# Kernel tuning notes

Hardware: AMD Instinct MI355X
Metric: run time of the kernel (lower is better)

Reference implementation:

```python
import jax, jax.numpy as jnp
import numpy as np

N = 500_000
LEVELS = 3
GDIM = 8
BASE_H = 128
BASE_W = 128
COND = 64
DOUT = 128
HID = 2
DIN = 1 + 2 * LEVELS * GDIM  # rho + theta-grid feats + rho-grid feats = 49


def _bilinear(grid, u, v):
    # grid: [H, W, D]; u, v in [0,1]; u indexes W axis, v indexes H axis.
    H, W, D = grid.shape
    x = u * (W - 1)
    y = v * (H - 1)
    x0 = jnp.clip(jnp.floor(x).astype(jnp.int32), 0, W - 2)
    y0 = jnp.clip(jnp.floor(y).astype(jnp.int32), 0, H - 2)
    x1 = x0 + 1
    y1 = y0 + 1
    wx = (x - x0)[:, None]
    wy = (y - y0)[:, None]
    g = grid.reshape(H * W, D)
    c00 = jnp.take(g, y0 * W + x0, axis=0)
    c01 = jnp.take(g, y0 * W + x1, axis=0)
    c10 = jnp.take(g, y1 * W + x0, axis=0)
    c11 = jnp.take(g, y1 * W + x1, axis=0)
    return (c00 * (1 - wx) * (1 - wy) + c01 * wx * (1 - wy)
            + c10 * (1 - wx) * wy + c11 * wx * wy)


def setup_inputs() -> dict:
    key = jax.random.key(0)
    ks = jax.random.split(key, 24)
    inp = {
        'coords': jax.random.uniform(ks[0], (N,), dtype=jnp.float32),
        'angles': jax.random.uniform(ks[1], (N,), dtype=jnp.float32),
        'rho': jax.random.normal(ks[2], (N,), dtype=jnp.float32),
        'rho_n': jax.random.uniform(ks[3], (N,), dtype=jnp.float32),
        'curve_feats': jax.random.normal(ks[4], (N, COND), dtype=jnp.float32),
        'type_sample': jax.random.normal(ks[5], (N, DOUT), dtype=jnp.float32),
    }
    # Multi-resolution grids (theta-conditioned and rho-conditioned).
    for l in range(LEVELS):
        h, w = BASE_H * 2 ** l, BASE_W * 2 ** l
        inp[f'gt{l}'] = 0.1 * jax.random.normal(ks[6 + l], (h, w, GDIM), dtype=jnp.float32)
        inp[f'gr{l}'] = 0.1 * jax.random.normal(ks[9 + l], (h, w, GDIM), dtype=jnp.float32)
    # FiLM-modulated encoder chain (block 0 + HID residual blocks).
    inp['film0_fcW'] = jax.random.normal(ks[12], (DIN, DOUT), dtype=jnp.float32) / np.sqrt(DIN)
    inp['film0_fcb'] = jnp.zeros((DOUT,), dtype=jnp.float32)
    inp['filmh_fcW'] = jax.random.normal(ks[13], (HID, DOUT, DOUT), dtype=jnp.float32) / np.sqrt(DOUT)
    inp['filmh_fcb'] = jnp.zeros((HID, DOUT), dtype=jnp.float32)
    inp['gammaW'] = 0.02 * jax.random.normal(ks[14], (HID + 1, COND, DOUT), dtype=jnp.float32)
    inp['gammab'] = jnp.ones((HID + 1, DOUT), dtype=jnp.float32)
    inp['betaW'] = 0.02 * jax.random.normal(ks[15], (HID + 1, COND, DOUT), dtype=jnp.float32)
    inp['betab'] = jnp.zeros((HID + 1, DOUT), dtype=jnp.float32)
    # Decoder MLP [DOUT, 64, 1].
    inp['decW1'] = jax.random.normal(ks[16], (DOUT, 64), dtype=jnp.float32) / np.sqrt(DOUT)
    inp['decb1'] = jnp.zeros((64,), dtype=jnp.float32)
    inp['decW2'] = jax.random.normal(ks[17], (64, 1), dtype=jnp.float32) / 8.0
    inp['decb2'] = jnp.zeros((1,), dtype=jnp.float32)
    return inp


def reference(coords, angles, rho, rho_n, curve_feats, type_sample,
              gt0, gt1, gt2, gr0, gr1, gr2,
              film0_fcW, film0_fcb, filmh_fcW, filmh_fcb,
              gammaW, gammab, betaW, betab,
              decW1, decb1, decW2, decb2):
    # Multi-res grid interpolation, concat across levels.
    ct = jnp.concatenate([_bilinear(g, angles, coords) for g in (gt0, gt1, gt2)], axis=-1)
    cr = jnp.concatenate([_bilinear(g, rho_n, coords) for g in (gr0, gr1, gr2)], axis=-1)
    feat = jnp.concatenate([rho[:, None], ct, cr], axis=-1)  # [N, DIN]
    # FiLM conditioning: gamma/beta per block from curve_feats.
    gamma = jnp.einsum('nc,lcd->lnd', curve_feats, gammaW) + gammab[:, None, :]
    beta = jnp.einsum('nc,lcd->lnd', curve_feats, betaW) + betab[:, None, :]
    # Block 0 + type_sample residual.
    x = jax.nn.silu(gamma[0] * (feat @ film0_fcW + film0_fcb) + beta[0]) + type_sample
    # Residual FiLM blocks.
    for i in range(filmh_fcW.shape[0]):
        x = x + jax.nn.silu(gamma[i + 1] * (x @ filmh_fcW[i] + filmh_fcb[i]) + beta[i + 1])
    # Decoder MLP.
    h = jax.nn.relu(x @ decW1 + decb1)
    sdf = (h @ decW2 + decb2)[..., 0]  # [N]
    return sdf
```

## Files before the change

### kernel.cpp

```cpp
#include <hip/hip_runtime.h>
#include <stdint.h>

typedef short s16x8 __attribute__((ext_vector_type(8)));
typedef short s16x4 __attribute__((ext_vector_type(4)));
typedef float f32x4 __attribute__((ext_vector_type(4)));

#define MFMA16(a, b, c) __builtin_amdgcn_mfma_f32_16x16x32_bf16(a, b, c, 0, 0, 0)

__device__ __forceinline__ short f2bf(float f) {
  uint32_t u = __builtin_bit_cast(uint32_t, f);
  u += 0x7FFFu + ((u >> 16) & 1u);
  return (short)(u >> 16);
}

__global__ void pack_w(const float* __restrict__ w0, const float* __restrict__ wh,
                       const float* __restrict__ gw, const float* __restrict__ bw,
                       const float* __restrict__ d1, short* __restrict__ out) {
  int idx = blockIdx.x * 512 + threadIdx.x;
  if (idx >= 98304) return;
  int f = idx >> 9;
  int r = idx & 511;
  int lane = r >> 3, e = r & 7;
  int kk = ((lane >> 4) << 3) + e;
  int nn = lane & 15;
  float v;
  if (f < 16) {
    int ct = f >> 1, ks = f & 1;
    int k = ks * 32 + kk, n = ct * 16 + nn;
    if (k < 48) v = w0[(1 + k) * 128 + n];
    else if (k == 48) v = w0[n];
    else v = 0.f;
  } else if (f < 112) {
    int f2 = f - 16;
    int ks = f2 & 1, ct = (f2 >> 1) & 7, gb = (f2 >> 4) & 1, l = f2 >> 5;
    int k = ks * 32 + kk, n = ct * 16 + nn;
    const float* Wp = gb ? bw : gw;
    v = Wp[(l * 64 + k) * 128 + n];
  } else if (f < 176) {
    int f2 = f - 112;
    int ks = f2 & 3, ct = (f2 >> 2) & 7, i = f2 >> 5;
    int k = ks * 32 + kk, n = ct * 16 + nn;
    v = wh[(i * 128 + k) * 128 + n];
  } else {
    int f2 = f - 176;
    int ks = f2 & 3, ct = f2 >> 2;
    int k = ks * 32 + kk, n = ct * 16 + nn;
    v = d1[k * 64 + n];
  }
  out[idx] = f2bf(v);
}

__global__ __launch_bounds__(512) void ngc_main(
    const float* __restrict__ coords, const float* __restrict__ angles,
    const float* __restrict__ rho, const float* __restrict__ rho_n,
    const float* __restrict__ cf, const float* __restrict__ ts,
    const float* __restrict__ gt0, const float* __restrict__ gr0,
    const float* __restrict__ gt1, const float* __restrict__ gr1,
    const float* __restrict__ gt2, const float* __restrict__ gr2,
    const float* __restrict__ f0b, const float* __restrict__ fhb,
    const float* __restrict__ gab, const float* __restrict__ beb,
    const float* __restrict__ d1b, const float* __restrict__ d2w,
    const float* __restrict__ d2b, const short* __restrict__ pw,
    float* __restrict__ out, int n) {
  __shared__ __align__(16) char smem[33 * 1024];
  char* featA = smem;
  char* cfA   = smem + 8 * 1024;
  char* xA    = smem + 16 * 1024;
  float* red  = (float*)(smem + 32 * 1024);

  const int tid = threadIdx.x;
  const int lane = tid & 63;
  const int w = tid >> 6;
  const int g16 = lane >> 4;
  const int l15 = lane & 15;
  const int row0 = blockIdx.x * 64;
  const int col = w * 16 + l15;
  const int cbase = col >> 5;
  const int cslot = ((col >> 3) & 3) * 16;
  const int ce = (col & 7) * 2;

  float tsr[4][4];
#pragma unroll
  for (int rg = 0; rg < 4; ++rg)
#pragma unroll
    for (int rr = 0; rr < 4; ++rr) {
      int grow = row0 + rg * 16 + g16 * 4 + rr; grow = grow < n ? grow : n - 1;
      tsr[rg][rr] = ts[(size_t)grow * 128 + col];
    }

  if (tid < 384) {
    int r = tid & 63, g = tid >> 6;
    int gr_ = row0 + r; gr_ = gr_ < n ? gr_ : n - 1;
    float vv = coords[gr_];
    float u = (g < 3) ? angles[gr_] : rho_n[gr_];
    int lvl = (g < 3) ? g : g - 3;
    const float* G = (g == 0) ? gt0 : (g == 1) ? gt1 : (g == 2) ? gt2
                   : (g == 3) ? gr0 : (g == 4) ? gr1 : gr2;
    int Wg = 128 << lvl;
    float x = u * (float)(Wg - 1), y = vv * (float)(Wg - 1);
    int ix = (int)x; ix = ix < 0 ? 0 : (ix > Wg - 2 ? Wg - 2 : ix);
    int iy = (int)y; iy = iy < 0 ? 0 : (iy > Wg - 2 ? Wg - 2 : iy);
    float wx = x - (float)ix, wy = y - (float)iy;
    const float4* p0 = (const float4*)(G + (size_t)(iy * Wg + ix) * 8);
    const float4* p1 = (const float4*)(G + (size_t)((iy + 1) * Wg + ix) * 8);
    float4 c00a = p0[0], c00b = p0[1], c01a = p0[2], c01b = p0[3];
    float4 c10a = p1[0], c10b = p1[1], c11a = p1[2], c11b = p1[3];
    float w00 = (1.f - wx) * (1.f - wy), w01 = wx * (1.f - wy);
    float w10 = (1.f - wx) * wy, w11 = wx * wy;
    s16x8 o;
    o[0] = f2bf(c00a.x * w00 + c01a.x * w01 + c10a.x * w10 + c11a.x * w11);
    o[1] = f2bf(c00a.y * w00 + c01a.y * w01 + c10a.y * w10 + c11a.y * w11);
    o[2] = f2bf(c00a.z * w00 + c01a.z * w01 + c10a.z * w10 + c11a.z * w11);
    o[3] = f2bf(c00a.w * w00 + c01a.w * w01 + c10a.w * w10 + c11a.w * w11);
    o[4] = f2bf(c00b.x * w00 + c01b.x * w01 + c10b.x * w10 + c11b.x * w11);
    o[5] = f2bf(c00b.y * w00 + c01b.y * w01 + c10b.y * w10 + c11b.y * w11);
    o[6] = f2bf(c00b.z * w00 + c01b.z * w01 + c10b.z * w10 + c11b.z * w11);
    o[7] = f2bf(c00b.w * w00 + c01b.w * w01 + c10b.w * w10 + c11b.w * w11);
    int dst16 = ((r >> 4) * 2 + (g >> 2)) * 64 + (g & 3) * 16 + (r & 15);
    *(s16x8*)(featA + dst16 * 16) = o;
  }

  {
    int cb = tid & 7, r = tid >> 3;
    int gr_ = row0 + r; gr_ = gr_ < n ? gr_ : n - 1;
    const float4* cp = (const float4*)(cf + (size_t)gr_ * 64 + cb * 8);
    float4 v0 = cp[0], v1 = cp[1];
    s16x8 s = { f2bf(v0.x), f2bf(v0.y), f2bf(v0.z), f2bf(v0.w),
                f2bf(v1.x), f2bf(v1.y), f2bf(v1.z), f2bf(v1.w) };
    int dst16 = ((r >> 4) * 2 + (cb >> 2)) * 64 + (cb & 3) * 16 + (r & 15);
    *(s16x8*)(cfA + dst16 * 16) = s;
  }

  if (tid < 64) {
    int r = tid;
    int gr_ = row0 + r; gr_ = gr_ < n ? gr_ : n - 1;
    s16x8 a = { f2bf(rho[gr_]), 0, 0, 0, 0, 0, 0, 0 };
    s16x8 z = { 0, 0, 0, 0, 0, 0, 0, 0 };
    int base = ((r >> 4) * 2 + 1) * 64;
    *(s16x8*)(featA + (base + 32 + (r & 15)) * 16) = a;
    *(s16x8*)(featA + (base + 48 + (r & 15)) * 16) = z;
  }
  __syncthreads();

  auto ldF = [&](const char* b, int frag) -> s16x8 {
    return *(const s16x8*)(b + (frag * 64 + lane) * 16);
  };
  auto ldw = [&](int frag) -> s16x8 { return ((const s16x8*)pw)[frag * 64 + lane]; };

  float xr[4][4];

  {
    s16x8 bw0 = ldw(w * 2), bw1 = ldw(w * 2 + 1);
    s16x8 bg0 = ldw(16 + w * 2), bg1 = ldw(16 + w * 2 + 1);
    s16x8 bb0 = ldw(32 + w * 2), bb1 = ldw(32 + w * 2 + 1);
    float f0bv = f0b[col], gabv = gab[col], bebv = beb[col];
#pragma unroll
    for (int rg = 0; rg < 4; ++rg) {
      s16x8 a0 = ldF(featA, rg * 2), a1 = ldF(featA, rg * 2 + 1);
      s16x8 c0 = ldF(cfA, rg * 2), c1 = ldF(cfA, rg * 2 + 1);
      f32x4 t = {0.f, 0.f, 0.f, 0.f};
      t = MFMA16(a0, bw0, t); t = MFMA16(a1, bw1, t);
      f32x4 ga = {0.f, 0.f, 0.f, 0.f};
      ga = MFMA16(c0, bg0, ga); ga = MFMA16(c1, bg1, ga);
      f32x4 be = {0.f, 0.f, 0.f, 0.f};
      be = MFMA16(c0, bb0, be); be = MFMA16(c1, bb1, be);
      char* xbase = xA + (rg * 4 + cbase) * 1024 + ce;
#pragma unroll
      for (int rr = 0; rr < 4; ++rr) {
        float z = (ga[rr] + gabv) * (t[rr] + f0bv) + (be[rr] + bebv);
        float sl = z * __builtin_amdgcn_rcpf(1.f + __expf(-z));
        xr[rg][rr] = sl + tsr[rg][rr];
        *(short*)(xbase + (cslot + g16 * 4 + rr) * 16) = f2bf(xr[rg][rr]);
      }
    }
  }
  __syncthreads();

#pragma unroll
  for (int i = 0; i < 2; ++i) {
    s16x8 bh0 = ldw(112 + i * 32 + w * 4);
    s16x8 bh1 = ldw(112 + i * 32 + w * 4 + 1);
    s16x8 bh2 = ldw(112 + i * 32 + w * 4 + 2);
    s16x8 bh3 = ldw(112 + i * 32 + w * 4 + 3);
    s16x8 bg0 = ldw(16 + (i + 1) * 32 + w * 2);
    s16x8 bg1 = ldw(16 + (i + 1) * 32 + w * 2 + 1);
    s16x8 bb0 = ldw(16 + (i + 1) * 32 + 16 + w * 2);
    s16x8 bb1 = ldw(16 + (i + 1) * 32 + 16 + w * 2 + 1);
    float fhbv = fhb[i * 128 + col];
    float gabv = gab[(i + 1) * 128 + col];
    float bebv = beb[(i + 1) * 128 + col];
    f32x4 zs[4];
#pragma unroll
    for (int rg = 0; rg < 4; ++rg) {
      s16x8 xa = ldF(xA, rg * 4), xb = ldF(xA, rg * 4 + 1);
      s16x8 xc = ldF(xA, rg * 4 + 2), xd = ldF(xA, rg * 4 + 3);
      s16x8 c0 = ldF(cfA, rg * 2), c1 = ldF(cfA, rg * 2 + 1);
      f32x4 t = {0.f, 0.f, 0.f, 0.f};
      t = MFMA16(xa, bh0, t); t = MFMA16(xb, bh1, t);
      t = MFMA16(xc, bh2, t); t = MFMA16(xd, bh3, t);
      f32x4 ga = {0.f, 0.f, 0.f, 0.f};
      ga = MFMA16(c0, bg0, ga); ga = MFMA16(c1, bg1, ga);
      f32x4 be = {0.f, 0.f, 0.f, 0.f};
      be = MFMA16(c0, bb0, be); be = MFMA16(c1, bb1, be);
      f32x4 z;
#pragma unroll
      for (int rr = 0; rr < 4; ++rr) {
        float zz = (ga[rr] + gabv) * (t[rr] + fhbv) + (be[rr] + bebv);
        z[rr] = zz * __builtin_amdgcn_rcpf(1.f + __expf(-zz));
      }
      zs[rg] = z;
    }
    __syncthreads();
#pragma unroll
    for (int rg = 0; rg < 4; ++rg) {
      char* xbase = xA + (rg * 4 + cbase) * 1024 + ce;
#pragma unroll
      for (int rr = 0; rr < 4; ++rr) {
        xr[rg][rr] += zs[rg][rr];
        *(short*)(xbase + (cslot + g16 * 4 + rr) * 16) = f2bf(xr[rg][rr]);
      }
    }
    __syncthreads();
  }

  {
    int ctd = w & 3, rbase = (w >> 2) * 2;
    int dcol = ctd * 16 + l15;
    s16x8 bd0 = ldw(176 + ctd * 4), bd1 = ldw(176 + ctd * 4 + 1);
    s16x8 bd2 = ldw(176 + ctd * 4 + 2), bd3 = ldw(176 + ctd * 4 + 3);
    float d1bv = d1b[dcol], w2v = d2w[dcol];
#pragma unroll
    for (int q = 0; q < 2; ++q) {
      int rg = rbase + q;
      s16x8 xa = ldF(xA, rg * 4), xb = ldF(xA, rg * 4 + 1);
      s16x8 xc = ldF(xA, rg * 4 + 2), xd = ldF(xA, rg * 4 + 3);
      f32x4 hh = {0.f, 0.f, 0.f, 0.f};
      hh = MFMA16(xa, bd0, hh); hh = MFMA16(xb, bd1, hh);
      hh = MFMA16(xc, bd2, hh); hh = MFMA16(xd, bd3, hh);
#pragma unroll
      for (int rr = 0; rr < 4; ++rr) {
        float h = fmaxf(hh[rr] + d1bv, 0.f) * w2v;
        h += __shfl_xor(h, 1);
        h += __shfl_xor(h, 2);
        h += __shfl_xor(h, 4);
        h += __shfl_xor(h, 8);
        if (l15 == 0) red[(rg * 16 + g16 * 4 + rr) * 4 + ctd] = h;
      }
    }
  }
  __syncthreads();
  if (tid < 64) {
    int grow = row0 + tid;
    if (grow < n)
      out[grow] = red[tid * 4 + 0] + red[tid * 4 + 1] + red[tid * 4 + 2] +
                  red[tid * 4 + 3] + d2b[0];
  }
}

extern "C" void kernel_launch(void* const* d_in, const int* in_sizes, int n_in,
                              void* d_out, int out_size, void* d_ws, size_t ws_size,
                              hipStream_t stream) {
  int n = in_sizes[0];
  short* pw = (short*)d_ws;
  pack_w<<<192, 512, 0, stream>>>(
      (const float*)d_in[12],
      (const float*)d_in[14],
      (const float*)d_in[16],
      (const float*)d_in[18],
      (const float*)d_in[20],
      pw);
  int nb = (n + 63) / 64;
  ngc_main<<<nb, 512, 0, stream>>>(
      (const float*)d_in[0],
      (const float*)d_in[1],
      (const float*)d_in[2],
      (const float*)d_in[3],
      (const float*)d_in[4],
      (const float*)d_in[5],
      (const float*)d_in[6],
      (const float*)d_in[7],
      (const float*)d_in[8],
      (const float*)d_in[9],
      (const float*)d_in[10],
      (const float*)d_in[11],
      (const float*)d_in[13],
      (const float*)d_in[15],
      (const float*)d_in[17],
      (const float*)d_in[19],
      (const float*)d_in[21],
      (const float*)d_in[22],
      (const float*)d_in[23],
      pw, (float*)d_out, n);
}
```

Measured before the change: 259.6 us.

## Make main kernel persistent with register prefetch of next tile inputs

Launches a fixed grid of at most 512 blocks that stride over the 64-row tiles instead of one block per tile. While the current tile computes, each block loads the next tile's coordinates, angles, rho, curve features and type_sample rows into registers, so global latency overlaps with the MFMA stages. The cost is fewer resident blocks per CU, which means less latency hiding through occupancy, plus some load imbalance because the tile count does not divide evenly by the grid size. Register pressure also rises from holding the prefetched values.

Result: slower. 284.4 us (+9.6%).

```diff
diff --git a/kernel.cpp b/kernel.cpp
--- a/kernel.cpp
+++ b/kernel.cpp
@@ -2,10 +2,10 @@
 #include <stdint.h>
 
 typedef short s16x8 __attribute__((ext_vector_type(8)));
-typedef short s16x4 __attribute__((ext_vector_type(4)));
 typedef float f32x4 __attribute__((ext_vector_type(4)));
 
 #define MFMA16(a, b, c) __builtin_amdgcn_mfma_f32_16x16x32_bf16(a, b, c, 0, 0, 0)
+#define NBLK 512
 
 __device__ __forceinline__ short f2bf(float f) {
   uint32_t u = __builtin_bit_cast(uint32_t, f);
@@ -61,7 +61,7 @@
     const float* __restrict__ gab, const float* __restrict__ beb,
     const float* __restrict__ d1b, const float* __restrict__ d2w,
     const float* __restrict__ d2b, const short* __restrict__ pw,
-    float* __restrict__ out, int n) {
+    float* __restrict__ out, int n, int ntiles) {
   __shared__ __align__(16) char smem[33 * 1024];
   char* featA = smem;
   char* cfA   = smem + 8 * 1024;
@@ -73,187 +73,207 @@
   const int w = tid >> 6;
   const int g16 = lane >> 4;
   const int l15 = lane & 15;
-  const int row0 = blockIdx.x * 64;
   const int col = w * 16 + l15;
   const int cbase = col >> 5;
   const int cslot = ((col >> 3) & 3) * 16;
   const int ce = (col & 7) * 2;
 
+  const int r_g = tid & 63;
+  const int g_id = tid >> 6;
+  const int r_cf = tid >> 3;
+  const int cb = tid & 7;
+
+  float c_, a_, rn_, rhov;
+  float4 cf0, cf1;
   float tsr[4][4];
-#pragma unroll
-  for (int rg = 0; rg < 4; ++rg)
-#pragma unroll
-    for (int rr = 0; rr < 4; ++rr) {
-      int grow = row0 + rg * 16 + g16 * 4 + rr; grow = grow < n ? grow : n - 1;
-      tsr[rg][rr] = ts[(size_t)grow * 128 + col];
-    }
-
-  if (tid < 384) {
-    int r = tid & 63, g = tid >> 6;
-    int gr_ = row0 + r; gr_ = gr_ < n ? gr_ : n - 1;
-    float vv = coords[gr_];
-    float u = (g < 3) ? angles[gr_] : rho_n[gr_];
-    int lvl = (g < 3) ? g : g - 3;
-    const float* G = (g == 0) ? gt0 : (g == 1) ? gt1 : (g == 2) ? gt2
-                   : (g == 3) ? gr0 : (g == 4) ? gr1 : gr2;
-    int Wg = 128 << lvl;
-    float x = u * (float)(Wg - 1), y = vv * (float)(Wg - 1);
-    int ix = (int)x; ix = ix < 0 ? 0 : (ix > Wg - 2 ? Wg - 2 : ix);
-    int iy = (int)y; iy = iy < 0 ? 0 : (iy > Wg - 2 ? Wg - 2 : iy);
-    float wx = x - (float)ix, wy = y - (float)iy;
-    const float4* p0 = (const float4*)(G + (size_t)(iy * Wg + ix) * 8);
-    const float4* p1 = (const float4*)(G + (size_t)((iy + 1) * Wg + ix) * 8);
-    float4 c00a = p0[0], c00b = p0[1], c01a = p0[2], c01b = p0[3];
-    float4 c10a = p1[0], c10b = p1[1], c11a = p1[2], c11b = p1[3];
-    float w00 = (1.f - wx) * (1.f - wy), w01 = wx * (1.f - wy);
-    float w10 = (1.f - wx) * wy, w11 = wx * wy;
-    s16x8 o;
-    o[0] = f2bf(c00a.x * w00 + c01a.x * w01 + c10a.x * w10 + c11a.x * w11);
-    o[1] = f2bf(c00a.y * w00 + c01a.y * w01 + c10a.y * w10 + c11a.y * w11);
-    o[2] = f2bf(c00a.z * w00 + c01a.z * w01 + c10a.z * w10 + c11a.z * w11);
-    o[3] = f2bf(c00a.w * w00 + c01a.w * w01 + c10a.w * w10 + c11a.w * w11);
-    o[4] = f2bf(c00b.x * w00 + c01b.x * w01 + c10b.x * w10 + c11b.x * w11);
-    o[5] = f2bf(c00b.y * w00 + c01b.y * w01 + c10b.y * w10 + c11b.y * w11);
-    o[6] = f2bf(c00b.z * w00 + c01b.z * w01 + c10b.z * w10 + c11b.z * w11);
-    o[7] = f2bf(c00b.w * w00 + c01b.w * w01 + c10b.w * w10 + c11b.w * w11);
-    int dst16 = ((r >> 4) * 2 + (g >> 2)) * 64 + (g & 3) * 16 + (r & 15);
-    *(s16x8*)(featA + dst16 * 16) = o;
-  }
-
-  {
-    int cb = tid & 7, r = tid >> 3;
-    int gr_ = row0 + r; gr_ = gr_ < n ? gr_ : n - 1;
-    const float4* cp = (const float4*)(cf + (size_t)gr_ * 64 + cb * 8);
-    float4 v0 = cp[0], v1 = cp[1];
-    s16x8 s = { f2bf(v0.x), f2bf(v0.y), f2bf(v0.z), f2bf(v0.w),
-                f2bf(v1.x), f2bf(v1.y), f2bf(v1.z), f2bf(v1.w) };
-    int dst16 = ((r >> 4) * 2 + (cb >> 2)) * 64 + (cb & 3) * 16 + (r & 15);
-    *(s16x8*)(cfA + dst16 * 16) = s;
-  }
-
-  if (tid < 64) {
-    int r = tid;
-    int gr_ = row0 + r; gr_ = gr_ < n ? gr_ : n - 1;
-    s16x8 a = { f2bf(rho[gr_]), 0, 0, 0, 0, 0, 0, 0 };
-    s16x8 z = { 0, 0, 0, 0, 0, 0, 0, 0 };
-    int base = ((r >> 4) * 2 + 1) * 64;
-    *(s16x8*)(featA + (base + 32 + (r & 15)) * 16) = a;
-    *(s16x8*)(featA + (base + 48 + (r & 15)) * 16) = z;
-  }
-  __syncthreads();
+
+  auto issueA = [&](int tt) {
+    int row0 = tt * 64;
+    int gr1 = row0 + r_g; gr1 = gr1 < n ? gr1 : n - 1;
+    c_ = coords[gr1]; a_ = angles[gr1]; rn_ = rho_n[gr1]; rhov = rho[gr1];
+    int gr2 = row0 + r_cf; gr2 = gr2 < n ? gr2 : n - 1;
+    const float4* cp = (const float4*)(cf + (size_t)gr2 * 64 + cb * 8);
+    cf0 = cp[0]; cf1 = cp[1];
+  };
+  auto issueT = [&](int tt) {
+    int row0 = tt * 64;
+#pragma unroll
+    for (int rg = 0; rg < 4; ++rg)
+#pragma unroll
+      for (int rr = 0; rr < 4; ++rr) {
+        int grow = row0 + rg * 16 + g16 * 4 + rr; grow = grow < n ? grow : n - 1;
+        tsr[rg][rr] = ts[(size_t)grow * 128 + col];
+      }
+  };
 
   auto ldF = [&](const char* b, int frag) -> s16x8 {
     return *(const s16x8*)(b + (frag * 64 + lane) * 16);
   };
   auto ldw = [&](int frag) -> s16x8 { return ((const s16x8*)pw)[frag * 64 + lane]; };
 
-  float xr[4][4];
-
-  {
-    s16x8 bw0 = ldw(w * 2), bw1 = ldw(w * 2 + 1);
-    s16x8 bg0 = ldw(16 + w * 2), bg1 = ldw(16 + w * 2 + 1);
-    s16x8 bb0 = ldw(32 + w * 2), bb1 = ldw(32 + w * 2 + 1);
-    float f0bv = f0b[col], gabv = gab[col], bebv = beb[col];
-#pragma unroll
-    for (int rg = 0; rg < 4; ++rg) {
-      s16x8 a0 = ldF(featA, rg * 2), a1 = ldF(featA, rg * 2 + 1);
-      s16x8 c0 = ldF(cfA, rg * 2), c1 = ldF(cfA, rg * 2 + 1);
-      f32x4 t = {0.f, 0.f, 0.f, 0.f};
-      t = MFMA16(a0, bw0, t); t = MFMA16(a1, bw1, t);
-      f32x4 ga = {0.f, 0.f, 0.f, 0.f};
-      ga = MFMA16(c0, bg0, ga); ga = MFMA16(c1, bg1, ga);
-      f32x4 be = {0.f, 0.f, 0.f, 0.f};
-      be = MFMA16(c0, bb0, be); be = MFMA16(c1, bb1, be);
-      char* xbase = xA + (rg * 4 + cbase) * 1024 + ce;
-#pragma unroll
-      for (int rr = 0; rr < 4; ++rr) {
-        float z = (ga[rr] + gabv) * (t[rr] + f0bv) + (be[rr] + bebv);
-        float sl = z * __builtin_amdgcn_rcpf(1.f + __expf(-z));
-        xr[rg][rr] = sl + tsr[rg][rr];
-        *(short*)(xbase + (cslot + g16 * 4 + rr) * 16) = f2bf(xr[rg][rr]);
-      }
-    }
-  }
-  __syncthreads();
-
-#pragma unroll
-  for (int i = 0; i < 2; ++i) {
-    s16x8 bh0 = ldw(112 + i * 32 + w * 4);
-    s16x8 bh1 = ldw(112 + i * 32 + w * 4 + 1);
-    s16x8 bh2 = ldw(112 + i * 32 + w * 4 + 2);
-    s16x8 bh3 = ldw(112 + i * 32 + w * 4 + 3);
-    s16x8 bg0 = ldw(16 + (i + 1) * 32 + w * 2);
-    s16x8 bg1 = ldw(16 + (i + 1) * 32 + w * 2 + 1);
-    s16x8 bb0 = ldw(16 + (i + 1) * 32 + 16 + w * 2);
-    s16x8 bb1 = ldw(16 + (i + 1) * 32 + 16 + w * 2 + 1);
-    float fhbv = fhb[i * 128 + col];
-    float gabv = gab[(i + 1) * 128 + col];
-    float bebv = beb[(i + 1) * 128 + col];
-    f32x4 zs[4];
-#pragma unroll
-    for (int rg = 0; rg < 4; ++rg) {
-      s16x8 xa = ldF(xA, rg * 4), xb = ldF(xA, rg * 4 + 1);
-      s16x8 xc = ldF(xA, rg * 4 + 2), xd = ldF(xA, rg * 4 + 3);
-      s16x8 c0 = ldF(cfA, rg * 2), c1 = ldF(cfA, rg * 2 + 1);
-      f32x4 t = {0.f, 0.f, 0.f, 0.f};
-      t = MFMA16(xa, bh0, t); t = MFMA16(xb, bh1, t);
-      t = MFMA16(xc, bh2, t); t = MFMA16(xd, bh3, t);
-      f32x4 ga = {0.f, 0.f, 0.f, 0.f};
-      ga = MFMA16(c0, bg0, ga); ga = MFMA16(c1, bg1, ga);
-      f32x4 be = {0.f, 0.f, 0.f, 0.f};
-      be = MFMA16(c0, bb0, be); be = MFMA16(c1, bb1, be);
-      f32x4 z;
-#pragma unroll
-      for (int rr = 0; rr < 4; ++rr) {
-        float zz = (ga[rr] + gabv) * (t[rr] + fhbv) + (be[rr] + bebv);
-        z[rr] = zz * __builtin_amdgcn_rcpf(1.f + __expf(-zz));
-      }
-      zs[rg] = z;
-    }
+  int t = blockIdx.x;
+  issueA(t);
+  issueT(t);
+
+  for (; t < ntiles; t += NBLK) {
+    const int row0 = t * 64;
+
+    if (tid < 384) {
+      int r = r_g, g = g_id;
+      float u = (g < 3) ? a_ : rn_;
+      int lvl = (g < 3) ? g : g - 3;
+      const float* G = (g == 0) ? gt0 : (g == 1) ? gt1 : (g == 2) ? gt2
+                     : (g == 3) ? gr0 : (g == 4) ? gr1 : gr2;
+      int Wg = 128 << lvl;
+      float x = u * (float)(Wg - 1), y = c_ * (float)(Wg - 1);
+      int ix = (int)x; ix = ix < 0 ? 0 : (ix > Wg - 2 ? Wg - 2 : ix);
+      int iy = (int)y; iy = iy < 0 ? 0 : (iy > Wg - 2 ? Wg - 2 : iy);
+      float wx = x - (float)ix, wy = y - (float)iy;
+      const float4* p0 = (const float4*)(G + (size_t)(iy * Wg + ix) * 8);
+      const float4* p1 = (const float4*)(G + (size_t)((iy + 1) * Wg + ix) * 8);
+      float4 c00a = p0[0], c00b = p0[1], c01a = p0[2], c01b = p0[3];
+      float4 c10a = p1[0], c10b = p1[1], c11a = p1[2], c11b = p1[3];
+      float w00 = (1.f - wx) * (1.f - wy), w01 = wx * (1.f - wy);
+      float w10 = (1.f - wx) * wy, w11 = wx * wy;
+      s16x8 o;
+      o[0] = f2bf(c00a.x * w00 + c01a.x * w01 + c10a.x * w10 + c11a.x * w11);
+      o[1] = f2bf(c00a.y * w00 + c01a.y * w01 + c10a.y * w10 + c11a.y * w11);
+      o[2] = f2bf(c00a.z * w00 + c01a.z * w01 + c10a.z * w10 + c11a.z * w11);
+      o[3] = f2bf(c00a.w * w00 + c01a.w * w01 + c10a.w * w10 + c11a.w * w11);
+      o[4] = f2bf(c00b.x * w00 + c01b.x * w01 + c10b.x * w10 + c11b.x * w11);
+      o[5] = f2bf(c00b.y * w00 + c01b.y * w01 + c10b.y * w10 + c11b.y * w11);
+      o[6] = f2bf(c00b.z * w00 + c01b.z * w01 + c10b.z * w10 + c11b.z * w11);
+      o[7] = f2bf(c00b.w * w00 + c01b.w * w01 + c10b.w * w10 + c11b.w * w11);
+      int dst16 = ((r >> 4) * 2 + (g >> 2)) * 64 + (g & 3) * 16 + (r & 15);
+      *(s16x8*)(featA + dst16 * 16) = o;
+    }
+    {
+      s16x8 s = { f2bf(cf0.x), f2bf(cf0.y), f2bf(cf0.z), f2bf(cf0.w),
+                  f2bf(cf1.x), f2bf(cf1.y), f2bf(cf1.z), f2bf(cf1.w) };
+      int dst16 = ((r_cf >> 4) * 2 + (cb >> 2)) * 64 + (cb & 3) * 16 + (r_cf & 15);
+      *(s16x8*)(cfA + dst16 * 16) = s;
+    }
+    if (tid < 64) {
+      int r = tid;
+      s16x8 a = { f2bf(rhov), 0, 0, 0, 0, 0, 0, 0 };
+      s16x8 z = { 0, 0, 0, 0, 0, 0, 0, 0 };
+      int base = ((r >> 4) * 2 + 1) * 64;
+      *(s16x8*)(featA + (base + 32 + (r & 15)) * 16) = a;
+      *(s16x8*)(featA + (base + 48 + (r & 15)) * 16) = z;
+    }
+    int tn = t + NBLK;
+    if (tn < ntiles) issueA(tn);
     __syncthreads();
-#pragma unroll
-    for (int rg = 0; rg < 4; ++rg) {
-      char* xbase = xA + (rg * 4 + cbase) * 1024 + ce;
-#pragma unroll
-      for (int rr = 0; rr < 4; ++rr) {
-        xr[rg][rr] += zs[rg][rr];
-        *(short*)(xbase + (cslot + g16 * 4 + rr) * 16) = f2bf(xr[rg][rr]);
-      }
-    }
+
+    float xr[4][4];
+
+    {
+      s16x8 bw0 = ldw(w * 2), bw1 = ldw(w * 2 + 1);
+      s16x8 bg0 = ldw(16 + w * 2), bg1 = ldw(16 + w * 2 + 1);
+      s16x8 bb0 = ldw(32 + w * 2), bb1 = ldw(32 + w * 2 + 1);
+      float f0bv = f0b[col], gabv = gab[col], bebv = beb[col];
+#pragma unroll
+      for (int rg = 0; rg < 4; ++rg) {
+        s16x8 a0 = ldF(featA, rg * 2), a1 = ldF(featA, rg * 2 + 1);
+        s16x8 c0 = ldF(cfA, rg * 2), c1 = ldF(cfA, rg * 2 + 1);
+        f32x4 tt = {0.f, 0.f, 0.f, 0.f};
+        tt = MFMA16(a0, bw0, tt); tt = MFMA16(a1, bw1, tt);
+        f32x4 ga = {0.f, 0.f, 0.f, 0.f};
+        ga = MFMA16(c0, bg0, ga); ga = MFMA16(c1, bg1, ga);
+        f32x4 be = {0.f, 0.f, 0.f, 0.f};
+        be = MFMA16(c0, bb0, be); be = MFMA16(c1, bb1, be);
+        char* xbase = xA + (rg * 4 + cbase) * 1024 + ce;
+#pragma unroll
+        for (int rr = 0; rr < 4; ++rr) {
+          float z = (ga[rr] + gabv) * (tt[rr] + f0bv) + (be[rr] + bebv);
+          float sl = z * __builtin_amdgcn_rcpf(1.f + __expf(-z));
+          xr[rg][rr] = sl + tsr[rg][rr];
+          *(short*)(xbase + (cslot + g16 * 4 + rr) * 16) = f2bf(xr[rg][rr]);
+        }
+      }
+    }
+    if (tn < ntiles) issueT(tn);
     __syncthreads();
-  }
-
-  {
-    int ctd = w & 3, rbase = (w >> 2) * 2;
-    int dcol = ctd * 16 + l15;
-    s16x8 bd0 = ldw(176 + ctd * 4), bd1 = ldw(176 + ctd * 4 + 1);
-    s16x8 bd2 = ldw(176 + ctd * 4 + 2), bd3 = ldw(176 + ctd * 4 + 3);
-    float d1bv = d1b[dcol], w2v = d2w[dcol];
-#pragma unroll
-    for (int q = 0; q < 2; ++q) {
-      int rg = rbase + q;
-      s16x8 xa = ldF(xA, rg * 4), xb = ldF(xA, rg * 4 + 1);
-      s16x8 xc = ldF(xA, rg * 4 + 2), xd = ldF(xA, rg * 4 + 3);
-      f32x4 hh = {0.f, 0.f, 0.f, 0.f};
-      hh = MFMA16(xa, bd0, hh); hh = MFMA16(xb, bd1, hh);
-      hh = MFMA16(xc, bd2, hh); hh = MFMA16(xd, bd3, hh);
-#pragma unroll
-      for (int rr = 0; rr < 4; ++rr) {
-        float h = fmaxf(hh[rr] + d1bv, 0.f) * w2v;
-        h += __shfl_xor(h, 1);
-        h += __shfl_xor(h, 2);
-        h += __shfl_xor(h, 4);
-        h += __shfl_xor(h, 8);
-        if (l15 == 0) red[(rg * 16 + g16 * 4 + rr) * 4 + ctd] = h;
-      }
-    }
-  }
-  __syncthreads();
-  if (tid < 64) {
-    int grow = row0 + tid;
-    if (grow < n)
-      out[grow] = red[tid * 4 + 0] + red[tid * 4 + 1] + red[tid * 4 + 2] +
-                  red[tid * 4 + 3] + d2b[0];
+
+#pragma unroll
+    for (int i = 0; i < 2; ++i) {
+      s16x8 bh0 = ldw(112 + i * 32 + w * 4);
+      s16x8 bh1 = ldw(112 + i * 32 + w * 4 + 1);
+      s16x8 bh2 = ldw(112 + i * 32 + w * 4 + 2);
+      s16x8 bh3 = ldw(112 + i * 32 + w * 4 + 3);
+      s16x8 bg0 = ldw(16 + (i + 1) * 32 + w * 2);
+      s16x8 bg1 = ldw(16 + (i + 1) * 32 + w * 2 + 1);
+      s16x8 bb0 = ldw(16 + (i + 1) * 32 + 16 + w * 2);
+      s16x8 bb1 = ldw(16 + (i + 1) * 32 + 16 + w * 2 + 1);
+      float fhbv = fhb[i * 128 + col];
+      float gabv = gab[(i + 1) * 128 + col];
+      float bebv = beb[(i + 1) * 128 + col];
+      f32x4 zs[4];
+#pragma unroll
+      for (int rg = 0; rg < 4; ++rg) {
+        s16x8 xa = ldF(xA, rg * 4), xb = ldF(xA, rg * 4 + 1);
+        s16x8 xc = ldF(xA, rg * 4 + 2), xd = ldF(xA, rg * 4 + 3);
+        s16x8 c0 = ldF(cfA, rg * 2), c1 = ldF(cfA, rg * 2 + 1);
+        f32x4 tt = {0.f, 0.f, 0.f, 0.f};
+        tt = MFMA16(xa, bh0, tt); tt = MFMA16(xb, bh1, tt);
+        tt = MFMA16(xc, bh2, tt); tt = MFMA16(xd, bh3, tt);
+        f32x4 ga = {0.f, 0.f, 0.f, 0.f};
+        ga = MFMA16(c0, bg0, ga); ga = MFMA16(c1, bg1, ga);
+        f32x4 be = {0.f, 0.f, 0.f, 0.f};
+        be = MFMA16(c0, bb0, be); be = MFMA16(c1, bb1, be);
+        f32x4 z;
+#pragma unroll
+        for (int rr = 0; rr < 4; ++rr) {
+          float zz = (ga[rr] + gabv) * (tt[rr] + fhbv) + (be[rr] + bebv);
+          z[rr] = zz * __builtin_amdgcn_rcpf(1.f + __expf(-zz));
+        }
+        zs[rg] = z;
+      }
+      __syncthreads();
+#pragma unroll
+      for (int rg = 0; rg < 4; ++rg) {
+        char* xbase = xA + (rg * 4 + cbase) * 1024 + ce;
+#pragma unroll
+        for (int rr = 0; rr < 4; ++rr) {
+          xr[rg][rr] += zs[rg][rr];
+          *(short*)(xbase + (cslot + g16 * 4 + rr) * 16) = f2bf(xr[rg][rr]);
+        }
+      }
+      __syncthreads();
+    }
+
+    {
+      int ctd = w & 3, rbase = (w >> 2) * 2;
+      int dcol = ctd * 16 + l15;
+      s16x8 bd0 = ldw(176 + ctd * 4), bd1 = ldw(176 + ctd * 4 + 1);
+      s16x8 bd2 = ldw(176 + ctd * 4 + 2), bd3 = ldw(176 + ctd * 4 + 3);
+      float d1bv = d1b[dcol], w2v = d2w[dcol];
+#pragma unroll
+      for (int q = 0; q < 2; ++q) {
+        int rg = rbase + q;
+        s16x8 xa = ldF(xA, rg * 4), xb = ldF(xA, rg * 4 + 1);
+        s16x8 xc = ldF(xA, rg * 4 + 2), xd = ldF(xA, rg * 4 + 3);
+        f32x4 hh = {0.f, 0.f, 0.f, 0.f};
+        hh = MFMA16(xa, bd0, hh); hh = MFMA16(xb, bd1, hh);
+        hh = MFMA16(xc, bd2, hh); hh = MFMA16(xd, bd3, hh);
+#pragma unroll
+        for (int rr = 0; rr < 4; ++rr) {
+          float h = fmaxf(hh[rr] + d1bv, 0.f) * w2v;
+          h += __shfl_xor(h, 1);
+          h += __shfl_xor(h, 2);
+          h += __shfl_xor(h, 4);
+          h += __shfl_xor(h, 8);
+          if (l15 == 0) red[(rg * 16 + g16 * 4 + rr) * 4 + ctd] = h;
+        }
+      }
+    }
+    __syncthreads();
+    if (tid < 64) {
+      int grow = row0 + tid;
+      if (grow < n)
+        out[grow] = red[tid * 4 + 0] + red[tid * 4 + 1] + red[tid * 4 + 2] +
+                    red[tid * 4 + 3] + d2b[0];
+    }
   }
 }
 
@@ -269,7 +289,8 @@
       (const float*)d_in[18],
       (const float*)d_in[20],
       pw);
-  int nb = (n + 63) / 64;
+  int ntiles = (n + 63) / 64;
+  int nb = ntiles < NBLK ? ntiles : NBLK;
   ngc_main<<<nb, 512, 0, stream>>>(
       (const float*)d_in[0],
       (const float*)d_in[1],
@@ -290,5 +311,5 @@
       (const float*)d_in[21],
       (const float*)d_in[22],
       (const float*)d_in[23],
-      pw, (float*)d_out, n);
+      pw, (float*)d_out, n, ntiles);
 }
```

## Split grid gather into separate kernel staging bf16 features in workspace

Applied to the files above, without the earlier changes.

The fused kernel is split in two. One kernel does the bilinear grid gathers and writes bf16 feature fragments to a global workspace buffer; a second kernel reads them directly as MFMA operands and runs the FiLM/MLP GEMM chain. The launches are issued in chunks sized to the available workspace. The split is meant to separate the latency-bound random gathers from the MFMA work, freeing LDS and improving occupancy of each kernel. Separately, the manual bf16 rounding is replaced with the packed v_cvt_pk_bf16_f32 instruction. The cost is an extra global write and read of the features plus more kernel launches.

Measured after the change: 284.5 us. +9.6%, slower.

```diff
diff --git a/kernel.cpp b/kernel.cpp
--- a/kernel.cpp
+++ b/kernel.cpp
@@ -2,8 +2,8 @@
 #include <stdint.h>
 
 typedef short s16x8 __attribute__((ext_vector_type(8)));
-typedef short s16x4 __attribute__((ext_vector_type(4)));
 typedef float f32x4 __attribute__((ext_vector_type(4)));
+typedef uint32_t u32x4 __attribute__((ext_vector_type(4)));
 
 #define MFMA16(a, b, c) __builtin_amdgcn_mfma_f32_16x16x32_bf16(a, b, c, 0, 0, 0)
 
@@ -12,6 +12,12 @@
   u += 0x7FFFu + ((u >> 16) & 1u);
   return (short)(u >> 16);
 }
+__device__ __forceinline__ uint32_t cvtpk(float lo, float hi) {
+  uint32_t r;
+  asm("v_cvt_pk_bf16_f32 %0, %1, %2" : "=v"(r) : "v"(lo), "v"(hi));
+  return r;
+}
+__device__ __forceinline__ short f2bf1(float f) { return (short)cvtpk(f, f); }
 
 __global__ void pack_w(const float* __restrict__ w0, const float* __restrict__ wh,
                        const float* __restrict__ gw, const float* __restrict__ bw,
@@ -50,43 +56,16 @@
   out[idx] = f2bf(v);
 }
 
-__global__ __launch_bounds__(512) void ngc_main(
+__global__ __launch_bounds__(512) void ngc_gather(
     const float* __restrict__ coords, const float* __restrict__ angles,
     const float* __restrict__ rho, const float* __restrict__ rho_n,
-    const float* __restrict__ cf, const float* __restrict__ ts,
     const float* __restrict__ gt0, const float* __restrict__ gr0,
     const float* __restrict__ gt1, const float* __restrict__ gr1,
     const float* __restrict__ gt2, const float* __restrict__ gr2,
-    const float* __restrict__ f0b, const float* __restrict__ fhb,
-    const float* __restrict__ gab, const float* __restrict__ beb,
-    const float* __restrict__ d1b, const float* __restrict__ d2w,
-    const float* __restrict__ d2b, const short* __restrict__ pw,
-    float* __restrict__ out, int n) {
-  __shared__ __align__(16) char smem[33 * 1024];
-  char* featA = smem;
-  char* cfA   = smem + 8 * 1024;
-  char* xA    = smem + 16 * 1024;
-  float* red  = (float*)(smem + 32 * 1024);
-
+    short* __restrict__ stage, int n, int t0) {
   const int tid = threadIdx.x;
-  const int lane = tid & 63;
-  const int w = tid >> 6;
-  const int g16 = lane >> 4;
-  const int l15 = lane & 15;
-  const int row0 = blockIdx.x * 64;
-  const int col = w * 16 + l15;
-  const int cbase = col >> 5;
-  const int cslot = ((col >> 3) & 3) * 16;
-  const int ce = (col & 7) * 2;
-
-  float tsr[4][4];
-#pragma unroll
-  for (int rg = 0; rg < 4; ++rg)
-#pragma unroll
-    for (int rr = 0; rr < 4; ++rr) {
-      int grow = row0 + rg * 16 + g16 * 4 + rr; grow = grow < n ? grow : n - 1;
-      tsr[rg][rr] = ts[(size_t)grow * 128 + col];
-    }
+  const int row0 = (t0 + blockIdx.x) * 64;
+  char* st = (char*)(stage + (size_t)blockIdx.x * 4096);
 
   if (tid < 384) {
     int r = tid & 63, g = tid >> 6;
@@ -107,41 +86,77 @@
     float4 c10a = p1[0], c10b = p1[1], c11a = p1[2], c11b = p1[3];
     float w00 = (1.f - wx) * (1.f - wy), w01 = wx * (1.f - wy);
     float w10 = (1.f - wx) * wy, w11 = wx * wy;
-    s16x8 o;
-    o[0] = f2bf(c00a.x * w00 + c01a.x * w01 + c10a.x * w10 + c11a.x * w11);
-    o[1] = f2bf(c00a.y * w00 + c01a.y * w01 + c10a.y * w10 + c11a.y * w11);
-    o[2] = f2bf(c00a.z * w00 + c01a.z * w01 + c10a.z * w10 + c11a.z * w11);
-    o[3] = f2bf(c00a.w * w00 + c01a.w * w01 + c10a.w * w10 + c11a.w * w11);
-    o[4] = f2bf(c00b.x * w00 + c01b.x * w01 + c10b.x * w10 + c11b.x * w11);
-    o[5] = f2bf(c00b.y * w00 + c01b.y * w01 + c10b.y * w10 + c11b.y * w11);
-    o[6] = f2bf(c00b.z * w00 + c01b.z * w01 + c10b.z * w10 + c11b.z * w11);
-    o[7] = f2bf(c00b.w * w00 + c01b.w * w01 + c10b.w * w10 + c11b.w * w11);
+    float e0 = c00a.x * w00 + c01a.x * w01 + c10a.x * w10 + c11a.x * w11;
+    float e1 = c00a.y * w00 + c01a.y * w01 + c10a.y * w10 + c11a.y * w11;
+    float e2 = c00a.z * w00 + c01a.z * w01 + c10a.z * w10 + c11a.z * w11;
+    float e3 = c00a.w * w00 + c01a.w * w01 + c10a.w * w10 + c11a.w * w11;
+    float e4 = c00b.x * w00 + c01b.x * w01 + c10b.x * w10 + c11b.x * w11;
+    float e5 = c00b.y * w00 + c01b.y * w01 + c10b.y * w10 + c11b.y * w11;
+    float e6 = c00b.z * w00 + c01b.z * w01 + c10b.z * w10 + c11b.z * w11;
+    float e7 = c00b.w * w00 + c01b.w * w01 + c10b.w * w10 + c11b.w * w11;
+    u32x4 o = { cvtpk(e0, e1), cvtpk(e2, e3), cvtpk(e4, e5), cvtpk(e6, e7) };
     int dst16 = ((r >> 4) * 2 + (g >> 2)) * 64 + (g & 3) * 16 + (r & 15);
-    *(s16x8*)(featA + dst16 * 16) = o;
-  }
+    *(u32x4*)(st + dst16 * 16) = o;
+  } else if (tid < 448) {
+    int r = tid - 384;
+    int gr_ = row0 + r; gr_ = gr_ < n ? gr_ : n - 1;
+    s16x8 a = { f2bf1(rho[gr_]), 0, 0, 0, 0, 0, 0, 0 };
+    int base = ((r >> 4) * 2 + 1) * 64;
+    *(s16x8*)(st + (base + 32 + (r & 15)) * 16) = a;
+  } else {
+    int r = tid - 448;
+    s16x8 z = { 0, 0, 0, 0, 0, 0, 0, 0 };
+    int base = ((r >> 4) * 2 + 1) * 64;
+    *(s16x8*)(st + (base + 48 + (r & 15)) * 16) = z;
+  }
+}
+
+__global__ __launch_bounds__(512) void ngc_gemm(
+    const float* __restrict__ cf, const float* __restrict__ ts,
+    const float* __restrict__ f0b, const float* __restrict__ fhb,
+    const float* __restrict__ gab, const float* __restrict__ beb,
+    const float* __restrict__ d1b, const float* __restrict__ d2w,
+    const float* __restrict__ d2b, const short* __restrict__ pw,
+    const short* __restrict__ stage, float* __restrict__ out, int n, int t0) {
+  __shared__ __align__(16) char smem[25 * 1024];
+  char* cfA = smem;
+  char* xA  = smem + 8 * 1024;
+  float* red = (float*)(smem + 24 * 1024);
+
+  const int tid = threadIdx.x;
+  const int lane = tid & 63;
+  const int w = tid >> 6;
+  const int g16 = lane >> 4;
+  const int l15 = lane & 15;
+  const int row0 = (t0 + blockIdx.x) * 64;
+  const int col = w * 16 + l15;
+  const int cbase = col >> 5;
+  const int cslot = ((col >> 3) & 3) * 16;
+  const int ce = (col & 7) * 2;
+
+  float tsr[4][4];
+#pragma unroll
+  for (int rg = 0; rg < 4; ++rg)
+#pragma unroll
+    for (int rr = 0; rr < 4; ++rr) {
+      int grow = row0 + rg * 16 + g16 * 4 + rr; grow = grow < n ? grow : n - 1;
+      tsr[rg][rr] = ts[(size_t)grow * 128 + col];
+    }
 
   {
     int cb = tid & 7, r = tid >> 3;
     int gr_ = row0 + r; gr_ = gr_ < n ? gr_ : n - 1;
     const float4* cp = (const float4*)(cf + (size_t)gr_ * 64 + cb * 8);
     float4 v0 = cp[0], v1 = cp[1];
-    s16x8 s = { f2bf(v0.x), f2bf(v0.y), f2bf(v0.z), f2bf(v0.w),
-                f2bf(v1.x), f2bf(v1.y), f2bf(v1.z), f2bf(v1.w) };
+    u32x4 s = { cvtpk(v0.x, v0.y), cvtpk(v0.z, v0.w),
+                cvtpk(v1.x, v1.y), cvtpk(v1.z, v1.w) };
     int dst16 = ((r >> 4) * 2 + (cb >> 2)) * 64 + (cb & 3) * 16 + (r & 15);
-    *(s16x8*)(cfA + dst16 * 16) = s;
-  }
-
-  if (tid < 64) {
-    int r = tid;
-    int gr_ = row0 + r; gr_ = gr_ < n ? gr_ : n - 1;
-    s16x8 a = { f2bf(rho[gr_]), 0, 0, 0, 0, 0, 0, 0 };
-    s16x8 z = { 0, 0, 0, 0, 0, 0, 0, 0 };
-    int base = ((r >> 4) * 2 + 1) * 64;
-    *(s16x8*)(featA + (base + 32 + (r & 15)) * 16) = a;
-    *(s16x8*)(featA + (base + 48 + (r & 15)) * 16) = z;
+    *(u32x4*)(cfA + dst16 * 16) = s;
   }
   __syncthreads();
 
+  const s16x8* fB = (const s16x8*)stage + (size_t)blockIdx.x * 512;
+  auto ldfeat = [&](int frag) -> s16x8 { return fB[frag * 64 + lane]; };
   auto ldF = [&](const char* b, int frag) -> s16x8 {
     return *(const s16x8*)(b + (frag * 64 + lane) * 16);
   };
@@ -156,7 +171,7 @@
     float f0bv = f0b[col], gabv = gab[col], bebv = beb[col];
 #pragma unroll
     for (int rg = 0; rg < 4; ++rg) {
-      s16x8 a0 = ldF(featA, rg * 2), a1 = ldF(featA, rg * 2 + 1);
+      s16x8 a0 = ldfeat(rg * 2), a1 = ldfeat(rg * 2 + 1);
       s16x8 c0 = ldF(cfA, rg * 2), c1 = ldF(cfA, rg * 2 + 1);
       f32x4 t = {0.f, 0.f, 0.f, 0.f};
       t = MFMA16(a0, bw0, t); t = MFMA16(a1, bw1, t);
@@ -170,7 +185,7 @@
         float z = (ga[rr] + gabv) * (t[rr] + f0bv) + (be[rr] + bebv);
         float sl = z * __builtin_amdgcn_rcpf(1.f + __expf(-z));
         xr[rg][rr] = sl + tsr[rg][rr];
-        *(short*)(xbase + (cslot + g16 * 4 + rr) * 16) = f2bf(xr[rg][rr]);
+        *(short*)(xbase + (cslot + g16 * 4 + rr) * 16) = f2bf1(xr[rg][rr]);
       }
     }
   }
@@ -217,7 +232,7 @@
 #pragma unroll
       for (int rr = 0; rr < 4; ++rr) {
         xr[rg][rr] += zs[rg][rr];
-        *(short*)(xbase + (cslot + g16 * 4 + rr) * 16) = f2bf(xr[rg][rr]);
+        *(short*)(xbase + (cslot + g16 * 4 + rr) * 16) = f2bf1(xr[rg][rr]);
       }
     }
     __syncthreads();
@@ -262,6 +277,14 @@
                               hipStream_t stream) {
   int n = in_sizes[0];
   short* pw = (short*)d_ws;
+  const size_t stage_off = 256 * 1024;
+  short* stage = (short*)((char*)d_ws + stage_off);
+  int ntiles = (n + 63) / 64;
+  long long avail = (long long)ws_size - (long long)stage_off;
+  int chunk = (int)(avail > 8192 ? avail / 8192 : 1);
+  if (chunk > ntiles) chunk = ntiles;
+  if (chunk < 1) chunk = 1;
+
   pack_w<<<192, 512, 0, stream>>>(
       (const float*)d_in[12],
       (const float*)d_in[14],
@@ -269,26 +292,31 @@
       (const float*)d_in[18],
       (const float*)d_in[20],
       pw);
-  int nb = (n + 63) / 64;
-  ngc_main<<<nb, 512, 0, stream>>>(
-      (const float*)d_in[0],
-      (const float*)d_in[1],
-      (const float*)d_in[2],
-      (const float*)d_in[3],
-      (const float*)d_in[4],
-      (const float*)d_in[5],
-      (const float*)d_in[6],
-      (const float*)d_in[7],
-      (const float*)d_in[8],
-      (const float*)d_in[9],
-      (const float*)d_in[10],
-      (const float*)d_in[11],
-      (const float*)d_in[13],
-      (const float*)d_in[15],
-      (const float*)d_in[17],
-      (const float*)d_in[19],
-      (const float*)d_in[21],
-      (const float*)d_in[22],
-      (const float*)d_in[23],
-      pw, (float*)d_out, n);
-}
+
+  for (int t0 = 0; t0 < ntiles; t0 += chunk) {
+    int nb = ntiles - t0 < chunk ? ntiles - t0 : chunk;
+    ngc_gather<<<nb, 512, 0, stream>>>(
+        (const float*)d_in[0],
+        (const float*)d_in[1],
+        (const float*)d_in[2],
+        (const float*)d_in[3],
+        (const float*)d_in[6],
+        (const float*)d_in[7],
+        (const float*)d_in[8],
+        (const float*)d_in[9],
+        (const float*)d_in[10],
+        (const float*)d_in[11],
+        stage, n, t0);
+    ngc_gemm<<<nb, 512, 0, stream>>>(
+        (const float*)d_in[4],
+        (const float*)d_in[5],
+        (const float*)d_in[13],
+        (const float*)d_in[15],
+        (const float*)d_in[17],
+        (const float*)d_in[19],
+        (const float*)d_in[21],
+        (const float*)d_in[22],
+        (const float*)d_in[23],
+        pw, stage, (float*)d_out, n, t0);
+  }
+}
```
